# Optimization experiments

Measured on AMD Instinct MI355X. Metric: run time of the kernel, lower is better.

## Reference

```python
import jax, jax.numpy as jnp
import numpy as np

B = 8192
IN_FEATURES = 4096
OUT_FEATURES = 4096
SRC = 64   # src_blocks
DST = 64   # dst_blocks
NB = IN_FEATURES // SRC  # 64 blocks


def setup_inputs() -> dict:
    key = jax.random.key(0)
    kx, kb = jax.random.split(key)
    x = jax.random.normal(kx, (B, IN_FEATURES), dtype=jnp.float32)
    # stacked block-diagonal parameters: [num_blocks, dst_blocks, src_blocks]
    blocks = jax.random.normal(kb, (NB, DST, SRC), dtype=jnp.float32)
    return {"x": x, "blocks": blocks}


def reference(x, blocks):
    # Block-diagonal linear: equivalent to assembling a dense
    # [out_features, in_features] weight with blocks on the diagonal and
    # applying nn.functional.linear, but computed as a batched block GEMM.
    nb, dst, src = blocks.shape
    xb = x.reshape(x.shape[0], nb, src)          # [B, nb, src]
    yb = jnp.einsum('bns,nds->bnd', xb, blocks)  # [B, nb, dst]
    return yb.reshape(x.shape[0], nb * dst)      # [B, out_features]
```

## Files before the change

### kernel.cpp

```cpp
#include <hip/hip_runtime.h>


#define NBLK 64
#define BLKD 64
#define INF 4096
#define NROWS 8192
#define CHUNK_ROWS 64
#define CHUNKS 4

typedef short bf16x8 __attribute__((ext_vector_type(8)));
typedef float f32x4 __attribute__((ext_vector_type(4)));

__device__ inline unsigned short bf_rne(float f) {
    union { float f; unsigned u; } v;
    v.f = f;
    unsigned u = v.u;
    u += 0x7fffu + ((u >> 16) & 1u);
    return (unsigned short)(u >> 16);
}

__device__ inline bf16x8 cvt8(float4 a, float4 b) {
    bf16x8 r;
    r[0] = (short)bf_rne(a.x);
    r[1] = (short)bf_rne(a.y);
    r[2] = (short)bf_rne(a.z);
    r[3] = (short)bf_rne(a.w);
    r[4] = (short)bf_rne(b.x);
    r[5] = (short)bf_rne(b.y);
    r[6] = (short)bf_rne(b.z);
    r[7] = (short)bf_rne(b.w);
    return r;
}

__global__ __launch_bounds__(256, 4) void StructuredLinearBlocks_kernel(
        const float* __restrict__ x, const float* __restrict__ w,
        float* __restrict__ y) {
    const int n    = blockIdx.y;
    const int tid  = threadIdx.x;
    const int wid  = tid >> 6;
    const int lane = tid & 63;
    const int l15  = lane & 15;
    const int lhi  = lane >> 4;

    const float* wn = w + n * (BLKD * BLKD);
    bf16x8 bfrag[4][2];
#pragma unroll
    for (int t = 0; t < 4; ++t) {
#pragma unroll
        for (int h = 0; h < 2; ++h) {
            const float* p = wn + (t * 16 + l15) * BLKD + h * 32 + lhi * 8;
            float4 lo = *(const float4*)p;
            float4 hi = *(const float4*)(p + 4);
            bfrag[t][h] = cvt8(lo, hi);
        }
    }

    const int row_wg = blockIdx.x * (CHUNK_ROWS * CHUNKS);
#pragma unroll
    for (int c = 0; c < CHUNKS; ++c) {
        const int r0 = row_wg + c * CHUNK_ROWS + wid * 16;

        const float* xp = x + (r0 + l15) * INF + n * BLKD;
        float4 a0 = *(const float4*)(xp + lhi * 8);
        float4 a1 = *(const float4*)(xp + lhi * 8 + 4);
        float4 a2 = *(const float4*)(xp + 32 + lhi * 8);
        float4 a3 = *(const float4*)(xp + 32 + lhi * 8 + 4);
        bf16x8 af0 = cvt8(a0, a1);
        bf16x8 af1 = cvt8(a2, a3);

        f32x4 acc[4];
#pragma unroll
        for (int t = 0; t < 4; ++t) {
            acc[t] = (f32x4){0.f, 0.f, 0.f, 0.f};
            acc[t] = __builtin_amdgcn_mfma_f32_16x16x32_bf16(af0, bfrag[t][0], acc[t], 0, 0, 0);
            acc[t] = __builtin_amdgcn_mfma_f32_16x16x32_bf16(af1, bfrag[t][1], acc[t], 0, 0, 0);
        }

        float* yp = y + (r0 + lhi * 4) * INF + n * BLKD + l15;
#pragma unroll
        for (int t = 0; t < 4; ++t) {
#pragma unroll
            for (int j = 0; j < 4; ++j) {
                yp[j * INF + t * 16] = acc[t][j];
            }
        }
    }
}

extern "C" void kernel_launch(void* const* d_in, const int* in_sizes, int n_in,
                              void* d_out, int out_size, void* d_ws, size_t ws_size,
                              hipStream_t stream) {
    const float* x = (const float*)d_in[0];
    const float* w = (const float*)d_in[1];
    float* y = (float*)d_out;

    dim3 grid(NROWS / (CHUNK_ROWS * CHUNKS), NBLK);
    dim3 block(256);
    StructuredLinearBlocks_kernel<<<grid, block, 0, stream>>>(x, w, y);
}
```

Before: 285.7 us.

## Stage x and weights through swizzled LDS with prefetch and vectorized transposed stores

Loads the weight block and each x chunk cooperatively with coalesced row-wise float4 reads, converts them to bf16 and stores them into XOR-swizzled LDS, from which MFMA fragments are read. The MFMA operands are swapped so each lane's accumulator holds consecutive output columns, which allows 16-byte vector stores instead of scalar strided stores. The next x chunk is prefetched into registers while the current one is computed. The cost is extra LDS traffic and two barriers per chunk, and the occupancy hint in the launch bounds is dropped.

```diff
diff --git a/kernel.cpp b/kernel.cpp
--- a/kernel.cpp
+++ b/kernel.cpp
@@ -21,68 +21,104 @@
 
 __device__ inline bf16x8 cvt8(float4 a, float4 b) {
     bf16x8 r;
-    r[0] = (short)bf_rne(a.x);
-    r[1] = (short)bf_rne(a.y);
-    r[2] = (short)bf_rne(a.z);
-    r[3] = (short)bf_rne(a.w);
-    r[4] = (short)bf_rne(b.x);
-    r[5] = (short)bf_rne(b.y);
-    r[6] = (short)bf_rne(b.z);
-    r[7] = (short)bf_rne(b.w);
+    r[0] = (short)bf_rne(a.x); r[1] = (short)bf_rne(a.y);
+    r[2] = (short)bf_rne(a.z); r[3] = (short)bf_rne(a.w);
+    r[4] = (short)bf_rne(b.x); r[5] = (short)bf_rne(b.y);
+    r[6] = (short)bf_rne(b.z); r[7] = (short)bf_rne(b.w);
     return r;
 }
 
-__global__ __launch_bounds__(256, 4) void StructuredLinearBlocks_kernel(
+__device__ inline int swz(int row, int colbyte) {
+    return row * 128 + (colbyte ^ ((row & 7) << 4));
+}
+
+__global__ __launch_bounds__(256) void StructuredLinearBlocks_kernel(
         const float* __restrict__ x, const float* __restrict__ w,
         float* __restrict__ y) {
-    const int n    = blockIdx.y;
+    __shared__ alignas(16) char lds[16384];
+    char* wl = lds;
+    char* xl = lds + 8192;
+
     const int tid  = threadIdx.x;
     const int wid  = tid >> 6;
     const int lane = tid & 63;
     const int l15  = lane & 15;
     const int lhi  = lane >> 4;
 
+    const int n = blockIdx.y;
     const float* wn = w + n * (BLKD * BLKD);
-    bf16x8 bfrag[4][2];
+    const int row_wg = blockIdx.x * (CHUNK_ROWS * CHUNKS);
+
+    const int srow = tid >> 3;
+    const int scol = (tid & 7) * 8;
+    const int wb0 = swz(srow,      scol * 2);
+    const int wb1 = swz(srow + 32, scol * 2);
+
+    float4 wr0a, wr0b, wr1a, wr1b;
+    {
+        const float* p0 = wn + (srow)      * BLKD + scol;
+        const float* p1 = wn + (srow + 32) * BLKD + scol;
+        wr0a = *(const float4*)p0; wr0b = *(const float4*)(p0 + 4);
+        wr1a = *(const float4*)p1; wr1b = *(const float4*)(p1 + 4);
+    }
+    float4 xr0a, xr0b, xr1a, xr1b;
+    {
+        const float* p0 = x + (row_wg + srow)      * INF + n * BLKD + scol;
+        const float* p1 = x + (row_wg + srow + 32) * INF + n * BLKD + scol;
+        xr0a = *(const float4*)p0; xr0b = *(const float4*)(p0 + 4);
+        xr1a = *(const float4*)p1; xr1b = *(const float4*)(p1 + 4);
+    }
+    *(bf16x8*)(wl + wb0) = cvt8(wr0a, wr0b);
+    *(bf16x8*)(wl + wb1) = cvt8(wr1a, wr1b);
+    *(bf16x8*)(xl + wb0) = cvt8(xr0a, xr0b);
+    *(bf16x8*)(xl + wb1) = cvt8(xr1a, xr1b);
+    __syncthreads();
+
+    bf16x8 bw[4][2];
 #pragma unroll
     for (int t = 0; t < 4; ++t) {
 #pragma unroll
         for (int h = 0; h < 2; ++h) {
-            const float* p = wn + (t * 16 + l15) * BLKD + h * 32 + lhi * 8;
-            float4 lo = *(const float4*)p;
-            float4 hi = *(const float4*)(p + 4);
-            bfrag[t][h] = cvt8(lo, hi);
+            bw[t][h] = *(const bf16x8*)(wl + swz(t * 16 + l15, h * 64 + lhi * 16));
         }
     }
 
-    const int row_wg = blockIdx.x * (CHUNK_ROWS * CHUNKS);
 #pragma unroll
     for (int c = 0; c < CHUNKS; ++c) {
-        const int r0 = row_wg + c * CHUNK_ROWS + wid * 16;
+        float4 na0, na1, nb0, nb1;
+        if (c < CHUNKS - 1) {
+            const float* p0 = x + (row_wg + (c + 1) * CHUNK_ROWS + srow)      * INF + n * BLKD + scol;
+            const float* p1 = x + (row_wg + (c + 1) * CHUNK_ROWS + srow + 32) * INF + n * BLKD + scol;
+            na0 = *(const float4*)p0; na1 = *(const float4*)(p0 + 4);
+            nb0 = *(const float4*)p1; nb1 = *(const float4*)(p1 + 4);
+        }
 
-        const float* xp = x + (r0 + l15) * INF + n * BLKD;
-        float4 a0 = *(const float4*)(xp + lhi * 8);
-        float4 a1 = *(const float4*)(xp + lhi * 8 + 4);
-        float4 a2 = *(const float4*)(xp + 32 + lhi * 8);
-        float4 a3 = *(const float4*)(xp + 32 + lhi * 8 + 4);
-        bf16x8 af0 = cvt8(a0, a1);
-        bf16x8 af1 = cvt8(a2, a3);
+        bf16x8 xa[2];
+#pragma unroll
+        for (int h = 0; h < 2; ++h) {
+            xa[h] = *(const bf16x8*)(xl + swz(wid * 16 + l15, h * 64 + lhi * 16));
+        }
 
         f32x4 acc[4];
 #pragma unroll
         for (int t = 0; t < 4; ++t) {
             acc[t] = (f32x4){0.f, 0.f, 0.f, 0.f};
-            acc[t] = __builtin_amdgcn_mfma_f32_16x16x32_bf16(af0, bfrag[t][0], acc[t], 0, 0, 0);
-            acc[t] = __builtin_amdgcn_mfma_f32_16x16x32_bf16(af1, bfrag[t][1], acc[t], 0, 0, 0);
+            acc[t] = __builtin_amdgcn_mfma_f32_16x16x32_bf16(bw[t][0], xa[0], acc[t], 0, 0, 0);
+            acc[t] = __builtin_amdgcn_mfma_f32_16x16x32_bf16(bw[t][1], xa[1], acc[t], 0, 0, 0);
         }
 
-        float* yp = y + (r0 + lhi * 4) * INF + n * BLKD + l15;
+        float* yp = y + (row_wg + c * CHUNK_ROWS + wid * 16 + l15) * INF
+                      + n * BLKD + lhi * 4;
 #pragma unroll
         for (int t = 0; t < 4; ++t) {
-#pragma unroll
-            for (int j = 0; j < 4; ++j) {
-                yp[j * INF + t * 16] = acc[t][j];
-            }
+            *(f32x4*)(yp + t * 16) = acc[t];
+        }
+
+        if (c < CHUNKS - 1) {
+            __syncthreads();
+            *(bf16x8*)(xl + wb0) = cvt8(na0, na1);
+            *(bf16x8*)(xl + wb1) = cvt8(nb0, nb1);
+            __syncthreads();
         }
     }
 }
```

After: 284.2 us. No clear change (-0.5%).

## Stage x and weights in swizzled LDS, double-buffer weights, coalesce output stores

Applied to the files above, without the earlier changes.

Each workgroup now handles 16 rows across 8 consecutive diagonal blocks. It stages the x tile and the weight blocks as bf16 in XOR-swizzled LDS, and double-buffers the next weight block's loads while computing the current one. Output goes through LDS so each row writes contiguous float4 stores instead of strided scalar stores. This should improve global load and store coalescing, at the cost of 48KB of LDS per workgroup, lower occupancy, extra barriers, and weights reloaded per 16-row tile.

```diff
diff --git a/kernel.cpp b/kernel.cpp
--- a/kernel.cpp
+++ b/kernel.cpp
@@ -1,89 +1,130 @@
 #include <hip/hip_runtime.h>
 
 
-#define NBLK 64
-#define BLKD 64
 #define INF 4096
 #define NROWS 8192
-#define CHUNK_ROWS 64
-#define CHUNKS 4
+#define ROWS_WG 16
+#define GN 8
 
 typedef short bf16x8 __attribute__((ext_vector_type(8)));
+typedef short bf16x4 __attribute__((ext_vector_type(4)));
 typedef float f32x4 __attribute__((ext_vector_type(4)));
 
 __device__ inline unsigned short bf_rne(float f) {
-    union { float f; unsigned u; } v;
-    v.f = f;
+    union { float f; unsigned u; } v; v.f = f;
     unsigned u = v.u;
     u += 0x7fffu + ((u >> 16) & 1u);
     return (unsigned short)(u >> 16);
 }
 
-__device__ inline bf16x8 cvt8(float4 a, float4 b) {
-    bf16x8 r;
-    r[0] = (short)bf_rne(a.x);
-    r[1] = (short)bf_rne(a.y);
-    r[2] = (short)bf_rne(a.z);
-    r[3] = (short)bf_rne(a.w);
-    r[4] = (short)bf_rne(b.x);
-    r[5] = (short)bf_rne(b.y);
-    r[6] = (short)bf_rne(b.z);
-    r[7] = (short)bf_rne(b.w);
+__device__ inline bf16x4 cvt4(float4 a) {
+    bf16x4 r;
+    r[0] = (short)bf_rne(a.x); r[1] = (short)bf_rne(a.y);
+    r[2] = (short)bf_rne(a.z); r[3] = (short)bf_rne(a.w);
     return r;
 }
 
-__global__ __launch_bounds__(256, 4) void StructuredLinearBlocks_kernel(
+__device__ inline int swzx(int row, int colbyte) {
+    return row * 1024 + (colbyte ^ ((row & 7) << 4));
+}
+__device__ inline int swzw(int row, int colbyte) {
+    return row * 128 + (colbyte ^ ((row & 7) << 4));
+}
+
+__global__ __launch_bounds__(256, 3) void StructuredLinearBlocks_kernel(
         const float* __restrict__ x, const float* __restrict__ w,
         float* __restrict__ y) {
-    const int n    = blockIdx.y;
+    __shared__ alignas(16) char lds[49152];
+    char* xp   = lds;
+    char* wbuf = lds + 16384;
+    char* ys   = lds + 32768;
+
     const int tid  = threadIdx.x;
     const int wid  = tid >> 6;
     const int lane = tid & 63;
     const int l15  = lane & 15;
     const int lhi  = lane >> 4;
 
-    const float* wn = w + n * (BLKD * BLKD);
-    bf16x8 bfrag[4][2];
+    const int bid = blockIdx.x;
+    const int g   = bid & 7;
+    const int p   = bid >> 3;
+    const int r0  = p * ROWS_WG;
+    const int n0  = g * GN;
+
+    {
+        float4 xv[4][2];
+        const float* xb = x + (size_t)r0 * INF + n0 * 64;
 #pragma unroll
-    for (int t = 0; t < 4; ++t) {
+        for (int r = 0; r < 4; ++r) {
+            const float* pr = xb + (size_t)((tid >> 6) + r * 4) * INF + (tid & 63) * 4;
+            xv[r][0] = *(const float4*)pr;
+            xv[r][1] = *(const float4*)(pr + 256);
+        }
+        float4 wv[4];
+        const float* pw = w + n0 * 4096 + tid * 4;
 #pragma unroll
-        for (int h = 0; h < 2; ++h) {
-            const float* p = wn + (t * 16 + l15) * BLKD + h * 32 + lhi * 8;
-            float4 lo = *(const float4*)p;
-            float4 hi = *(const float4*)(p + 4);
-            bfrag[t][h] = cvt8(lo, hi);
+        for (int k = 0; k < 4; ++k) wv[k] = *(const float4*)(pw + k * 1024);
+
+#pragma unroll
+        for (int r = 0; r < 4; ++r) {
+            int row = (tid >> 6) + r * 4;
+            int cb  = (tid & 63) * 8;
+            *(bf16x4*)(xp + swzx(row, cb))       = cvt4(xv[r][0]);
+            *(bf16x4*)(xp + swzx(row, cb + 512)) = cvt4(xv[r][1]);
         }
+        int wrow = tid >> 4, wcb = (tid & 15) * 8;
+#pragma unroll
+        for (int k = 0; k < 4; ++k)
+            *(bf16x4*)(wbuf + swzw(wrow + k * 16, wcb)) = cvt4(wv[k]);
     }
+    __syncthreads();
 
-    const int row_wg = blockIdx.x * (CHUNK_ROWS * CHUNKS);
+    f32x4 acc[4];
 #pragma unroll
-    for (int c = 0; c < CHUNKS; ++c) {
-        const int r0 = row_wg + c * CHUNK_ROWS + wid * 16;
-
-        const float* xp = x + (r0 + l15) * INF + n * BLKD;
-        float4 a0 = *(const float4*)(xp + lhi * 8);
-        float4 a1 = *(const float4*)(xp + lhi * 8 + 4);
-        float4 a2 = *(const float4*)(xp + 32 + lhi * 8);
-        float4 a3 = *(const float4*)(xp + 32 + lhi * 8 + 4);
-        bf16x8 af0 = cvt8(a0, a1);
-        bf16x8 af1 = cvt8(a2, a3);
-
-        f32x4 acc[4];
-#pragma unroll
-        for (int t = 0; t < 4; ++t) {
-            acc[t] = (f32x4){0.f, 0.f, 0.f, 0.f};
-            acc[t] = __builtin_amdgcn_mfma_f32_16x16x32_bf16(af0, bfrag[t][0], acc[t], 0, 0, 0);
-            acc[t] = __builtin_amdgcn_mfma_f32_16x16x32_bf16(af1, bfrag[t][1], acc[t], 0, 0, 0);
+    for (int i = 0; i < GN; ++i) {
+        float4 wv0, wv1, wv2, wv3;
+        if (i < GN - 1) {
+            const float* pw = w + (n0 + i + 1) * 4096 + tid * 4;
+            wv0 = *(const float4*)pw;
+            wv1 = *(const float4*)(pw + 1024);
+            wv2 = *(const float4*)(pw + 2048);
+            wv3 = *(const float4*)(pw + 3072);
         }
 
-        float* yp = y + (r0 + lhi * 4) * INF + n * BLKD + l15;
+        bf16x8 xa0 = *(const bf16x8*)(xp + swzx(l15, i * 128 + lhi * 16));
+        bf16x8 xa1 = *(const bf16x8*)(xp + swzx(l15, i * 128 + 64 + lhi * 16));
+        const char* wc = wbuf + (i & 1) * 8192;
+        bf16x8 bw0 = *(const bf16x8*)(wc + swzw(wid * 16 + l15, lhi * 16));
+        bf16x8 bw1 = *(const bf16x8*)(wc + swzw(wid * 16 + l15, 64 + lhi * 16));
+
+        f32x4 a = (f32x4){0.f, 0.f, 0.f, 0.f};
+        a = __builtin_amdgcn_mfma_f32_16x16x32_bf16(bw0, xa0, a, 0, 0, 0);
+        a = __builtin_amdgcn_mfma_f32_16x16x32_bf16(bw1, xa1, a, 0, 0, 0);
+        acc[i & 3] = a;
+
+        if ((i & 3) == 3) {
 #pragma unroll
-        for (int t = 0; t < 4; ++t) {
+            for (int j = 0; j < 4; ++j)
+                *(f32x4*)(ys + swzx(l15, j * 256 + wid * 64 + lhi * 16)) = acc[j];
+            __syncthreads();
+            const int gq = i >> 2;
 #pragma unroll
-            for (int j = 0; j < 4; ++j) {
-                yp[j * INF + t * 16] = acc[t][j];
+            for (int q = 0; q < 4; ++q) {
+                int r = wid * 4 + q;
+                f32x4 v = *(const f32x4*)(ys + swzx(r, lane * 16));
+                *(f32x4*)(y + (size_t)(r0 + r) * INF + (n0 + gq * 4) * 64 + lane * 4) = v;
             }
         }
+
+        if (i < GN - 1) {
+            char* wn = wbuf + ((i + 1) & 1) * 8192;
+            int wrow = tid >> 4, wcb = (tid & 15) * 8;
+            *(bf16x4*)(wn + swzw(wrow,      wcb)) = cvt4(wv0);
+            *(bf16x4*)(wn + swzw(wrow + 16, wcb)) = cvt4(wv1);
+            *(bf16x4*)(wn + swzw(wrow + 32, wcb)) = cvt4(wv2);
+            *(bf16x4*)(wn + swzw(wrow + 48, wcb)) = cvt4(wv3);
+        }
+        __syncthreads();
     }
 }
 
@@ -94,7 +135,7 @@
     const float* w = (const float*)d_in[1];
     float* y = (float*)d_out;
 
-    dim3 grid(NROWS / (CHUNK_ROWS * CHUNKS), NBLK);
+    dim3 grid((NROWS / ROWS_WG) * (64 / GN));
     dim3 block(256);
     StructuredLinearBlocks_kernel<<<grid, block, 0, stream>>>(x, w, y);
 }
```

After: 234.9 us. 1.22x faster.

## Stage rows through swizzled LDS for coalesced loads/stores with prefetch

Applied to the files above, without the earlier changes.

Restructures the kernel so each workgroup owns four diagonal blocks (256 columns) and iterates over 16-row panels in a persistent loop. Each thread now loads x with fully coalesced float4 row reads and writes y the same way, converting x to bf16 in XOR-swizzled LDS and staging the results through LDS. The next panel is prefetched into registers while the current one computes. This removes the strided 16-row-by-32-byte global access pattern of the old version, at the cost of extra LDS traffic and three barriers per iteration. The grid drops to 1024 workgroups, so there are fewer waves in flight to hide memory latency.

```diff
diff --git a/kernel.cpp b/kernel.cpp
--- a/kernel.cpp
+++ b/kernel.cpp
@@ -1,89 +1,126 @@
 #include <hip/hip_runtime.h>
 
 
-#define NBLK 64
-#define BLKD 64
 #define INF 4096
 #define NROWS 8192
-#define CHUNK_ROWS 64
-#define CHUNKS 4
+#define RPP 16
+#define GN 4
+#define NG 16
+#define NS 64
+#define PP ((NROWS / RPP) / NS)
 
 typedef short bf16x8 __attribute__((ext_vector_type(8)));
+typedef short bf16x4 __attribute__((ext_vector_type(4)));
 typedef float f32x4 __attribute__((ext_vector_type(4)));
 
 __device__ inline unsigned short bf_rne(float f) {
-    union { float f; unsigned u; } v;
-    v.f = f;
+    union { float f; unsigned u; } v; v.f = f;
     unsigned u = v.u;
     u += 0x7fffu + ((u >> 16) & 1u);
     return (unsigned short)(u >> 16);
 }
 
+__device__ inline bf16x4 cvt4(float4 a) {
+    bf16x4 r;
+    r[0] = (short)bf_rne(a.x); r[1] = (short)bf_rne(a.y);
+    r[2] = (short)bf_rne(a.z); r[3] = (short)bf_rne(a.w);
+    return r;
+}
+
 __device__ inline bf16x8 cvt8(float4 a, float4 b) {
     bf16x8 r;
-    r[0] = (short)bf_rne(a.x);
-    r[1] = (short)bf_rne(a.y);
-    r[2] = (short)bf_rne(a.z);
-    r[3] = (short)bf_rne(a.w);
-    r[4] = (short)bf_rne(b.x);
-    r[5] = (short)bf_rne(b.y);
-    r[6] = (short)bf_rne(b.z);
-    r[7] = (short)bf_rne(b.w);
+    r[0] = (short)bf_rne(a.x); r[1] = (short)bf_rne(a.y);
+    r[2] = (short)bf_rne(a.z); r[3] = (short)bf_rne(a.w);
+    r[4] = (short)bf_rne(b.x); r[5] = (short)bf_rne(b.y);
+    r[6] = (short)bf_rne(b.z); r[7] = (short)bf_rne(b.w);
     return r;
 }
+
+__device__ inline int swzx(int row, int cb) { return row * 512  + (cb ^ ((row & 7) << 4)); }
+__device__ inline int swzy(int row, int cb) { return row * 1024 + (cb ^ ((row & 7) << 4)); }
 
 __global__ __launch_bounds__(256, 4) void StructuredLinearBlocks_kernel(
         const float* __restrict__ x, const float* __restrict__ w,
         float* __restrict__ y) {
-    const int n    = blockIdx.y;
+    __shared__ alignas(16) char lds[32768];
+    char* ys = lds + 16384;
+
     const int tid  = threadIdx.x;
     const int wid  = tid >> 6;
     const int lane = tid & 63;
     const int l15  = lane & 15;
     const int lhi  = lane >> 4;
 
-    const float* wn = w + n * (BLKD * BLKD);
-    bf16x8 bfrag[4][2];
+    const int bid = blockIdx.x;
+    const int g   = bid & (NG - 1);
+    const int s   = bid >> 4;
+    const int c0  = g * (GN * 64);
+
+    bf16x8 bw[GN][2];
 #pragma unroll
-    for (int t = 0; t < 4; ++t) {
+    for (int n = 0; n < GN; ++n) {
 #pragma unroll
         for (int h = 0; h < 2; ++h) {
-            const float* p = wn + (t * 16 + l15) * BLKD + h * 32 + lhi * 8;
-            float4 lo = *(const float4*)p;
-            float4 hi = *(const float4*)(p + 4);
-            bfrag[t][h] = cvt8(lo, hi);
+            const float* p = w + (size_t)(g * GN + n) * 4096
+                               + (wid * 16 + l15) * 64 + h * 32 + lhi * 8;
+            bw[n][h] = cvt8(*(const float4*)p, *(const float4*)(p + 4));
         }
     }
 
-    const int row_wg = blockIdx.x * (CHUNK_ROWS * CHUNKS);
+    float4 xv[4];
 #pragma unroll
-    for (int c = 0; c < CHUNKS; ++c) {
-        const int r0 = row_wg + c * CHUNK_ROWS + wid * 16;
+    for (int r = 0; r < 4; ++r) {
+        const size_t row = (size_t)s * RPP + r * 4 + wid;
+        xv[r] = *(const float4*)(x + row * INF + c0 + lane * 4);
+    }
+#pragma unroll
+    for (int r = 0; r < 4; ++r)
+        *(bf16x4*)(lds + swzx(r * 4 + wid, lane * 8)) = cvt4(xv[r]);
+    __syncthreads();
 
-        const float* xp = x + (r0 + l15) * INF + n * BLKD;
-        float4 a0 = *(const float4*)(xp + lhi * 8);
-        float4 a1 = *(const float4*)(xp + lhi * 8 + 4);
-        float4 a2 = *(const float4*)(xp + 32 + lhi * 8);
-        float4 a3 = *(const float4*)(xp + 32 + lhi * 8 + 4);
-        bf16x8 af0 = cvt8(a0, a1);
-        bf16x8 af1 = cvt8(a2, a3);
+#pragma unroll 1
+    for (int it = 0; it < PP; ++it) {
+        char* cur = lds + (it & 1) * 8192;
+        char* nxt = lds + ((it + 1) & 1) * 8192;
 
-        f32x4 acc[4];
+        if (it + 1 < PP) {
 #pragma unroll
-        for (int t = 0; t < 4; ++t) {
-            acc[t] = (f32x4){0.f, 0.f, 0.f, 0.f};
-            acc[t] = __builtin_amdgcn_mfma_f32_16x16x32_bf16(af0, bfrag[t][0], acc[t], 0, 0, 0);
-            acc[t] = __builtin_amdgcn_mfma_f32_16x16x32_bf16(af1, bfrag[t][1], acc[t], 0, 0, 0);
+            for (int r = 0; r < 4; ++r) {
+                const size_t row = (size_t)((it + 1) * NS + s) * RPP + r * 4 + wid;
+                xv[r] = *(const float4*)(x + row * INF + c0 + lane * 4);
+            }
         }
 
-        float* yp = y + (r0 + lhi * 4) * INF + n * BLKD + l15;
+        f32x4 acc[GN];
 #pragma unroll
-        for (int t = 0; t < 4; ++t) {
+        for (int n = 0; n < GN; ++n) {
+            bf16x8 xa0 = *(const bf16x8*)(cur + swzx(l15, n * 128 + lhi * 16));
+            bf16x8 xa1 = *(const bf16x8*)(cur + swzx(l15, n * 128 + 64 + lhi * 16));
+            f32x4 a = (f32x4){0.f, 0.f, 0.f, 0.f};
+            a = __builtin_amdgcn_mfma_f32_16x16x32_bf16(bw[n][0], xa0, a, 0, 0, 0);
+            a = __builtin_amdgcn_mfma_f32_16x16x32_bf16(bw[n][1], xa1, a, 0, 0, 0);
+            acc[n] = a;
+        }
+
+        __syncthreads();
 #pragma unroll
-            for (int j = 0; j < 4; ++j) {
-                yp[j * INF + t * 16] = acc[t][j];
-            }
+        for (int n = 0; n < GN; ++n)
+            *(f32x4*)(ys + swzy(l15, n * 256 + wid * 64 + lhi * 16)) = acc[n];
+        __syncthreads();
+        const size_t r0 = (size_t)(it * NS + s) * RPP;
+#pragma unroll
+        for (int q = 0; q < 4; ++q) {
+            const int r = wid * 4 + q;
+            f32x4 v = *(const f32x4*)(ys + swzy(r, lane * 16));
+            *(f32x4*)(y + (r0 + r) * INF + c0 + lane * 4) = v;
         }
+
+        if (it + 1 < PP) {
+#pragma unroll
+            for (int r = 0; r < 4; ++r)
+                *(bf16x4*)(nxt + swzx(r * 4 + wid, lane * 8)) = cvt4(xv[r]);
+        }
+        __syncthreads();
     }
 }
 
@@ -94,7 +131,7 @@
     const float* w = (const float*)d_in[1];
     float* y = (float*)d_out;
 
-    dim3 grid(NROWS / (CHUNK_ROWS * CHUNKS), NBLK);
+    dim3 grid(NG * NS);
     dim3 block(256);
     StructuredLinearBlocks_kernel<<<grid, block, 0, stream>>>(x, w, y);
 }
```

Result: faster. 229.7 us (-19.6%).
